# Kernel optimization log

Hardware: AMD Instinct MI355X
Metric: run time of the kernel (lower is better)

## Reference

```python
import jax, jax.numpy as jnp
import numpy as np

ALPHA = 0.2          # LeakyReLU negative slope
NEG_BIG = -9e15      # zero_vec value used before softmax masking


def setup_inputs() -> dict:
    key = jax.random.key(0)
    k1, k2, k3, k4, k5 = jax.random.split(key, 5)
    N, M, F, K = 2048, 8192, 1024, 10
    feature_matrix = jax.random.normal(k1, (N, F), dtype=jnp.float32)
    embed_matrix = jax.random.normal(k2, (M, F), dtype=jnp.float32)
    # Xavier-ish scaling for params
    weight = jax.random.normal(k3, (F, F), dtype=jnp.float32) * (1.0 / np.sqrt(F))
    a = jax.random.normal(k4, (2 * F, 1), dtype=jnp.float32) * (1.0 / np.sqrt(2 * F))
    neigh_idx = jax.random.randint(k5, (N, K), 0, M, dtype=jnp.int64)
    return {
        "feature_matrix": feature_matrix,
        "embed_matrix": embed_matrix,
        "weight": weight,
        "a": a,
        "neigh_idx": neigh_idx,
    }


def reference(feature_matrix, embed_matrix, weight, a, neigh_idx):
    # feature_matrix: [N, F] features of batch nodes
    # embed_matrix:   [M, F] features of unique sampled neighbors
    # neigh_idx:      [N, K] sampled neighbor columns (set semantics: dups collapse)
    N, F = feature_matrix.shape
    M = embed_matrix.shape[0]
    rows = jnp.arange(N)[:, None]
    mask = jnp.zeros((N, M), dtype=feature_matrix.dtype).at[rows, neigh_idx].set(1.0)

    # GAT kernel path
    hf = feature_matrix @ weight          # [N, F]
    he = embed_matrix @ weight            # [M, F]
    # e_ij = leakyrelu([h_i || h_j] . a) == leakyrelu(h_i.a1 + h_j.a2)
    a1 = a[:F, 0]
    a2 = a[F:, 0]
    e = (hf @ a1)[:, None] + (he @ a2)[None, :]          # [N, M]
    e = jnp.where(e > 0, e, ALPHA * e)                   # LeakyReLU(0.2)
    scores = jnp.where(mask > 0, e, NEG_BIG)
    attention = jax.nn.softmax(scores, axis=1)           # row softmax
    to_feats = attention @ he                            # [N, F]
    return to_feats
```

## Files before the change

kernel.cpp:

```cpp
#include <hip/hip_runtime.h>
#include <math.h>

#define ALPHA 0.2f
#define MAXK 10

typedef _Float16 half8 __attribute__((ext_vector_type(8)));
typedef _Float16 half4 __attribute__((ext_vector_type(4)));
typedef float f32x4 __attribute__((ext_vector_type(4)));

__device__ __forceinline__ void gload_lds16(const void* g, void* l) {
    __builtin_amdgcn_global_load_lds(
        (const __attribute__((address_space(1))) unsigned int*)g,
        (__attribute__((address_space(3))) unsigned int*)l, 16, 0, 0);
}

__device__ __forceinline__ float dot4(float4 a, float4 b) {
    return a.x * b.x + a.y * b.y + a.z * b.z + a.w * b.w;
}

__global__ __launch_bounds__(256) void prep_kernel(
    const float* __restrict__ W, const float* __restrict__ a,
    float* __restrict__ wa, _Float16* __restrict__ Wt, int F) {
    const int tid = threadIdx.x;
    const int nWa = F >> 2;

    if ((int)blockIdx.x >= nWa) {
        __shared__ float t[32][33];
        const int tb = blockIdx.x - nWa;
        const int tpr = F >> 5;
        const int bx = (tb % tpr) * 32;
        const int by = (tb / tpr) * 32;
        const int x = tid & 31, y = tid >> 5;
        for (int i2 = y; i2 < 32; i2 += 8)
            t[i2][x] = W[(size_t)(bx + i2) * F + by + x];
        __syncthreads();
        for (int i2 = y; i2 < 32; i2 += 8)
            Wt[(size_t)(by + i2) * F + bx + x] = (_Float16)t[x][i2];
        return;
    }

    int wave = (int)((blockIdx.x * blockDim.x + tid) >> 6);
    int lane = tid & 63;
    const float4* wr = reinterpret_cast<const float4*>(W + (size_t)wave * F);
    const float4* a1 = reinterpret_cast<const float4*>(a);
    const float4* a2 = reinterpret_cast<const float4*>(a + F);
    float acc1 = 0.f, acc2 = 0.f;
    int F4 = F >> 2;
    for (int c = lane; c < F4; c += 64) {
        float4 w = wr[c];
        acc1 += dot4(w, a1[c]);
        acc2 += dot4(w, a2[c]);
    }
    #pragma unroll
    for (int off = 32; off; off >>= 1) {
        acc1 += __shfl_down(acc1, off);
        acc2 += __shfl_down(acc2, off);
    }
    if (lane == 0) { wa[wave] = acc1; wa[F + wave] = acc2; }
}

__global__ __launch_bounds__(256) void mid_kernel(
    const float* __restrict__ feat, const float* __restrict__ embed,
    const int* __restrict__ nidx, const float* __restrict__ wa,
    _Float16* __restrict__ agg, int F) {
    const int tid = threadIdx.x;
    const int i = blockIdx.x;
    const int f = tid * 4;

    int idx[MAXK];
    bool dup[MAXK];
    #pragma unroll
    for (int k = 0; k < MAXK; k++) idx[k] = nidx[i * MAXK + k];
    #pragma unroll
    for (int k = 0; k < MAXK; k++) {
        bool d = false;
        #pragma unroll
        for (int p = 0; p < MAXK; p++)
            if (p < k) d |= (idx[p] == idx[k]);
        dup[k] = d;
    }

    float4 wa1 = *(const float4*)&wa[f];
    float4 wa2 = *(const float4*)&wa[F + f];
    float4 fv  = *(const float4*)&feat[(size_t)i * F + f];
    float a1p = dot4(fv, wa1);

    float4 rv[MAXK];
    float a2p[MAXK];
    #pragma unroll
    for (int k = 0; k < MAXK; k++) {
        rv[k] = *(const float4*)&embed[(size_t)idx[k] * F + f];
        a2p[k] = dot4(rv[k], wa2);
    }

    #pragma unroll
    for (int off = 32; off; off >>= 1) {
        a1p += __shfl_down(a1p, off);
        #pragma unroll
        for (int k = 0; k < MAXK; k++) a2p[k] += __shfl_down(a2p[k], off);
    }
    __shared__ float red[MAXK + 1][4];
    const int w = tid >> 6, l = tid & 63;
    if (l == 0) {
        red[0][w] = a1p;
        #pragma unroll
        for (int k = 0; k < MAXK; k++) red[k + 1][w] = a2p[k];
    }
    __syncthreads();

    float s1 = red[0][0] + red[0][1] + red[0][2] + red[0][3];
    float sc[MAXK];
    float m = -INFINITY;
    #pragma unroll
    for (int k = 0; k < MAXK; k++) {
        float v = s1 + red[k + 1][0] + red[k + 1][1] + red[k + 1][2] + red[k + 1][3];
        v = v > 0.f ? v : ALPHA * v;
        sc[k] = v;
        if (!dup[k]) m = fmaxf(m, v);
    }
    float sum = 0.f;
    #pragma unroll
    for (int k = 0; k < MAXK; k++) {
        sc[k] = dup[k] ? 0.f : expf(sc[k] - m);
        sum += sc[k];
    }
    float inv = 1.0f / sum;

    float4 o = make_float4(0.f, 0.f, 0.f, 0.f);
    #pragma unroll
    for (int k = 0; k < MAXK; k++) {
        float wk = sc[k] * inv;
        o.x += wk * rv[k].x;
        o.y += wk * rv[k].y;
        o.z += wk * rv[k].z;
        o.w += wk * rv[k].w;
    }
    half4 h = { (_Float16)o.x, (_Float16)o.y, (_Float16)o.z, (_Float16)o.w };
    *(half4*)&agg[(size_t)i * F + f] = h;
}

__global__ __launch_bounds__(256) void gemm_f16_kernel(
    const _Float16* __restrict__ A, const _Float16* __restrict__ Bt,
    float* __restrict__ C, int M, int N, int K) {
    __shared__ _Float16 As[2][64 * 128];
    __shared__ _Float16 Bs[2][64 * 128];
    const int tid = threadIdx.x;

    int bid = blockIdx.y * gridDim.x + blockIdx.x;
    int nwg = gridDim.x * gridDim.y;
    int cpx = nwg >> 3;
    int wg = (bid & 7) * cpx + (bid >> 3);
    const int m0 = (wg / gridDim.x) * 64;
    const int n0 = (wg % gridDim.x) * 64;

    const int l = tid & 63, wv = tid >> 6;
    const int wm = wv >> 1, wn = wv & 1;
    const int lrow = l & 15, kc = l >> 4;
    const int nt = K >> 7;

    f32x4 acc[2][2] = {};

    #define STAGE(bf, t)                                                            \
    do {                                                                            \
        int k0_ = (t) * 128;                                                        \
        _Pragma("unroll")                                                           \
        for (int j_ = 0; j_ < 4; j_++) {                                            \
            int u_ = wv * 256 + j_ * 64 + l;                                        \
            int row_ = u_ >> 4, slot_ = (u_ & 15) ^ (row_ & 7);                     \
            gload_lds16(&A[(size_t)(m0 + row_) * K + k0_ + slot_ * 8],              \
                        (void*)((char*)&As[bf][0] + u_ * 16));                      \
        }                                                                           \
        _Pragma("unroll")                                                           \
        for (int j_ = 0; j_ < 4; j_++) {                                            \
            int u_ = wv * 256 + j_ * 64 + l;                                        \
            int row_ = u_ >> 4, slot_ = (u_ & 15) ^ (row_ & 7);                     \
            gload_lds16(&Bt[(size_t)(n0 + row_) * K + k0_ + slot_ * 8],             \
                        (void*)((char*)&Bs[bf][0] + u_ * 16));                      \
        }                                                                           \
    } while (0)

    STAGE(0, 0);

    int buf = 0;
    for (int t = 0; t < nt; ++t) {
        if (t + 1 < nt) {
            STAGE(buf ^ 1, t + 1);
            asm volatile("s_waitcnt vmcnt(8)" ::: "memory");
        } else {
            asm volatile("s_waitcnt vmcnt(0)" ::: "memory");
        }
        __builtin_amdgcn_s_barrier();
        __builtin_amdgcn_sched_barrier(0);

        __builtin_amdgcn_s_setprio(1);
        #pragma unroll
        for (int ks = 0; ks < 4; ks++) {
            half8 av[2], bv[2];
            #pragma unroll
            for (int fq = 0; fq < 2; fq++) {
                int arow = wm * 32 + fq * 16 + lrow;
                int ag = (ks * 4 + kc) ^ (arow & 7);
                av[fq] = *(const half8*)((const char*)&As[buf][0] + arow * 256 + ag * 16);
                int brow = wn * 32 + fq * 16 + lrow;
                int bg = (ks * 4 + kc) ^ (brow & 7);
                bv[fq] = *(const half8*)((const char*)&Bs[buf][0] + brow * 256 + bg * 16);
            }
            #pragma unroll
            for (int fq = 0; fq < 2; fq++)
                #pragma unroll
                for (int g = 0; g < 2; g++)
                    acc[fq][g] = __builtin_amdgcn_mfma_f32_16x16x32_f16(
                        av[fq], bv[g], acc[fq][g], 0, 0, 0);
        }
        __builtin_amdgcn_s_setprio(0);

        __builtin_amdgcn_sched_barrier(0);
        __builtin_amdgcn_s_barrier();
        buf ^= 1;
    }
    #undef STAGE

    #pragma unroll
    for (int fq = 0; fq < 2; fq++)
        #pragma unroll
        for (int g = 0; g < 2; g++)
            #pragma unroll
            for (int r = 0; r < 4; r++)
                C[(size_t)(m0 + wm * 32 + fq * 16 + kc * 4 + r) * N
                  + n0 + wn * 32 + g * 16 + lrow] = acc[fq][g][r];
}

extern "C" void kernel_launch(void* const* d_in, const int* in_sizes, int n_in,
                              void* d_out, int out_size, void* d_ws, size_t ws_size,
                              hipStream_t stream) {
    const float* feat  = (const float*)d_in[0];
    const float* embed = (const float*)d_in[1];
    const float* W     = (const float*)d_in[2];
    const float* a     = (const float*)d_in[3];
    const int*   nidx  = (const int*)d_in[4];

    int F = in_sizes[3] / 2;
    int N = in_sizes[0] / F;
    int M = in_sizes[1] / F;

    float* ws = (float*)d_ws;
    float* wa = ws;
    _Float16* agg_f16 = (_Float16*)(wa + 2 * F);
    _Float16* wt_f16  = agg_f16 + (size_t)N * F;
    (void)M;

    {
        int nWa = F / 4;
        int nT  = (F / 32) * (F / 32);
        prep_kernel<<<nWa + nT, 256, 0, stream>>>(W, a, wa, wt_f16, F);
    }
    mid_kernel<<<N, 256, 0, stream>>>(feat, embed, nidx, wa, agg_f16, F);
    {
        dim3 grid(F / 64, N / 64);
        gemm_f16_kernel<<<grid, 256, 0, stream>>>(agg_f16, wt_f16, (float*)d_out, N, F, F);
    }
}
```

Before: 37.25 us.

## Overlap second-half aggregation with first-half GEMM in a combined kernel

Splits the rows into two halves. The first half is aggregated by mid_kernel. A combo kernel then runs the GEMM for the first half in some blocks while other blocks aggregate the second half, and a final GEMM covers the second half. The aim is to fill the machine by letting gather-bound aggregation and MFMA-bound GEMM run concurrently. The cost is an extra launch, and the combo kernel reserves 32KB of LDS per block, which may lower occupancy for the aggregation blocks.

```diff
diff --git a/kernel.cpp b/kernel.cpp
--- a/kernel.cpp
+++ b/kernel.cpp
@@ -17,13 +17,158 @@
 __device__ __forceinline__ float dot4(float4 a, float4 b) {
     return a.x * b.x + a.y * b.y + a.z * b.z + a.w * b.w;
 }
+
+
+__device__ __forceinline__ void mid_body(
+    int i, int tid, const float* __restrict__ feat, const float* __restrict__ embed,
+    const int* __restrict__ nidx, const float* __restrict__ wa,
+    _Float16* __restrict__ agg, int F, char* smem) {
+    const int f = tid * 4;
+    int idx[MAXK];
+    bool dup[MAXK];
+    #pragma unroll
+    for (int k = 0; k < MAXK; k++) idx[k] = nidx[i * MAXK + k];
+    #pragma unroll
+    for (int k = 0; k < MAXK; k++) {
+        bool d = false;
+        #pragma unroll
+        for (int p = 0; p < MAXK; p++)
+            if (p < k) d |= (idx[p] == idx[k]);
+        dup[k] = d;
+    }
+    float4 wa1 = *(const float4*)&wa[f];
+    float4 wa2 = *(const float4*)&wa[F + f];
+    float4 fv  = *(const float4*)&feat[(size_t)i * F + f];
+    float a1p = dot4(fv, wa1);
+    float4 rv[MAXK];
+    float a2p[MAXK];
+    #pragma unroll
+    for (int k = 0; k < MAXK; k++) {
+        rv[k] = *(const float4*)&embed[(size_t)idx[k] * F + f];
+        a2p[k] = dot4(rv[k], wa2);
+    }
+    #pragma unroll
+    for (int off = 32; off; off >>= 1) {
+        a1p += __shfl_down(a1p, off);
+        #pragma unroll
+        for (int k = 0; k < MAXK; k++) a2p[k] += __shfl_down(a2p[k], off);
+    }
+    float (*red)[4] = (float(*)[4])smem;
+    const int w = tid >> 6, l = tid & 63;
+    if (l == 0) {
+        red[0][w] = a1p;
+        #pragma unroll
+        for (int k = 0; k < MAXK; k++) red[k + 1][w] = a2p[k];
+    }
+    __syncthreads();
+    float s1 = red[0][0] + red[0][1] + red[0][2] + red[0][3];
+    float sc[MAXK];
+    float m = -INFINITY;
+    #pragma unroll
+    for (int k = 0; k < MAXK; k++) {
+        float v = s1 + red[k + 1][0] + red[k + 1][1] + red[k + 1][2] + red[k + 1][3];
+        v = v > 0.f ? v : ALPHA * v;
+        sc[k] = v;
+        if (!dup[k]) m = fmaxf(m, v);
+    }
+    float sum = 0.f;
+    #pragma unroll
+    for (int k = 0; k < MAXK; k++) {
+        sc[k] = dup[k] ? 0.f : expf(sc[k] - m);
+        sum += sc[k];
+    }
+    float inv = 1.0f / sum;
+    float4 o = make_float4(0.f, 0.f, 0.f, 0.f);
+    #pragma unroll
+    for (int k = 0; k < MAXK; k++) {
+        float wk = sc[k] * inv;
+        o.x += wk * rv[k].x;
+        o.y += wk * rv[k].y;
+        o.z += wk * rv[k].z;
+        o.w += wk * rv[k].w;
+    }
+    half4 h = { (_Float16)o.x, (_Float16)o.y, (_Float16)o.z, (_Float16)o.w };
+    *(half4*)&agg[(size_t)i * F + f] = h;
+}
+
+__device__ __forceinline__ void gemm64_body(
+    int m0, int n0, int tid, const _Float16* __restrict__ A,
+    const _Float16* __restrict__ Bt, float* __restrict__ C,
+    int K, int Nc, char* smem) {
+    char* AsB = smem;
+    char* BsB = smem + 16384;
+    const int l = tid & 63, wv = tid >> 6;
+    const int wm = wv >> 1, wn = wv & 1;
+    const int lrow = l & 15, kc = l >> 4;
+    const int srow = l >> 3;
+    const int sslot = (l & 7) ^ (srow & 7);
+    const int nt = K >> 6;
+    const int rg0 = wv * 2, rg1 = wv * 2 + 1;
+    f32x4 acc[2][2] = {};
+
+    #define GSTAGE(bf, t_)                                                         \
+    do {                                                                           \
+        int k0_ = (t_) * 64;                                                       \
+        gload_lds16(&A[(size_t)(m0 + rg0 * 8 + srow) * K + k0_ + sslot * 8],       \
+                    (void*)(AsB + (bf) * 8192 + rg0 * 1024 + l * 16));             \
+        gload_lds16(&A[(size_t)(m0 + rg1 * 8 + srow) * K + k0_ + sslot * 8],       \
+                    (void*)(AsB + (bf) * 8192 + rg1 * 1024 + l * 16));             \
+        gload_lds16(&Bt[(size_t)(n0 + rg0 * 8 + srow) * K + k0_ + sslot * 8],      \
+                    (void*)(BsB + (bf) * 8192 + rg0 * 1024 + l * 16));             \
+        gload_lds16(&Bt[(size_t)(n0 + rg1 * 8 + srow) * K + k0_ + sslot * 8],      \
+                    (void*)(BsB + (bf) * 8192 + rg1 * 1024 + l * 16));             \
+    } while (0)
+
+    GSTAGE(0, 0);
+    asm volatile("s_waitcnt vmcnt(0)" ::: "memory");
+    __syncthreads();
+
+    int buf = 0;
+    for (int t = 0; t < nt; ++t) {
+        if (t + 1 < nt) GSTAGE(buf ^ 1, t + 1);
+        half8 av[2][2], bv[2][2];
+        #pragma unroll
+        for (int ks = 0; ks < 2; ks++) {
+            #pragma unroll
+            for (int fq = 0; fq < 2; fq++) {
+                int arow = wm * 32 + fq * 16 + lrow;
+                int aslot = (ks * 4 + kc) ^ (arow & 7);
+                av[ks][fq] = *(const half8*)(AsB + buf * 8192 + arow * 128 + aslot * 16);
+                int brow = wn * 32 + fq * 16 + lrow;
+                int bslot = (ks * 4 + kc) ^ (brow & 7);
+                bv[ks][fq] = *(const half8*)(BsB + buf * 8192 + brow * 128 + bslot * 16);
+            }
+        }
+        #pragma unroll
+        for (int ks = 0; ks < 2; ks++)
+            #pragma unroll
+            for (int fq = 0; fq < 2; fq++)
+                #pragma unroll
+                for (int g2 = 0; g2 < 2; g2++)
+                    acc[fq][g2] = __builtin_amdgcn_mfma_f32_16x16x32_f16(
+                        av[ks][fq], bv[ks][g2], acc[fq][g2], 0, 0, 0);
+        asm volatile("s_waitcnt vmcnt(0)" ::: "memory");
+        __syncthreads();
+        buf ^= 1;
+    }
+    #undef GSTAGE
+
+    #pragma unroll
+    for (int fq = 0; fq < 2; fq++)
+        #pragma unroll
+        for (int g2 = 0; g2 < 2; g2++)
+            #pragma unroll
+            for (int r = 0; r < 4; r++)
+                C[(size_t)(m0 + wm * 32 + fq * 16 + kc * 4 + r) * Nc
+                  + n0 + wn * 32 + g2 * 16 + lrow] = acc[fq][g2][r];
+}
+
 
 __global__ __launch_bounds__(256) void prep_kernel(
     const float* __restrict__ W, const float* __restrict__ a,
     float* __restrict__ wa, _Float16* __restrict__ Wt, int F) {
     const int tid = threadIdx.x;
     const int nWa = F >> 2;
-
     if ((int)blockIdx.x >= nWa) {
         __shared__ float t[32][33];
         const int tb = blockIdx.x - nWa;
@@ -38,7 +183,6 @@
             Wt[(size_t)(by + i2) * F + bx + x] = (_Float16)t[x][i2];
         return;
     }
-
     int wave = (int)((blockIdx.x * blockDim.x + tid) >> 6);
     int lane = tid & 63;
     const float4* wr = reinterpret_cast<const float4*>(W + (size_t)wave * F);
@@ -63,85 +207,34 @@
     const float* __restrict__ feat, const float* __restrict__ embed,
     const int* __restrict__ nidx, const float* __restrict__ wa,
     _Float16* __restrict__ agg, int F) {
+    __shared__ __align__(16) char smem[192];
+    mid_body(blockIdx.x, threadIdx.x, feat, embed, nidx, wa, agg, F, smem);
+}
+
+__global__ __launch_bounds__(256) void combo_kernel(
+    const float* __restrict__ feat, const float* __restrict__ embed,
+    const int* __restrict__ nidx, const float* __restrict__ wa,
+    const _Float16* __restrict__ agg_c, _Float16* __restrict__ agg,
+    const _Float16* __restrict__ Wt, float* __restrict__ C, int F, int halfN) {
+    __shared__ __align__(16) char smem[32768];
     const int tid = threadIdx.x;
-    const int i = blockIdx.x;
-    const int f = tid * 4;
-
-    int idx[MAXK];
-    bool dup[MAXK];
-    #pragma unroll
-    for (int k = 0; k < MAXK; k++) idx[k] = nidx[i * MAXK + k];
-    #pragma unroll
-    for (int k = 0; k < MAXK; k++) {
-        bool d = false;
-        #pragma unroll
-        for (int p = 0; p < MAXK; p++)
-            if (p < k) d |= (idx[p] == idx[k]);
-        dup[k] = d;
-    }
-
-    float4 wa1 = *(const float4*)&wa[f];
-    float4 wa2 = *(const float4*)&wa[F + f];
-    float4 fv  = *(const float4*)&feat[(size_t)i * F + f];
-    float a1p = dot4(fv, wa1);
-
-    float4 rv[MAXK];
-    float a2p[MAXK];
-    #pragma unroll
-    for (int k = 0; k < MAXK; k++) {
-        rv[k] = *(const float4*)&embed[(size_t)idx[k] * F + f];
-        a2p[k] = dot4(rv[k], wa2);
-    }
-
-    #pragma unroll
-    for (int off = 32; off; off >>= 1) {
-        a1p += __shfl_down(a1p, off);
-        #pragma unroll
-        for (int k = 0; k < MAXK; k++) a2p[k] += __shfl_down(a2p[k], off);
-    }
-    __shared__ float red[MAXK + 1][4];
-    const int w = tid >> 6, l = tid & 63;
-    if (l == 0) {
-        red[0][w] = a1p;
-        #pragma unroll
-        for (int k = 0; k < MAXK; k++) red[k + 1][w] = a2p[k];
-    }
-    __syncthreads();
-
-    float s1 = red[0][0] + red[0][1] + red[0][2] + red[0][3];
-    float sc[MAXK];
-    float m = -INFINITY;
-    #pragma unroll
-    for (int k = 0; k < MAXK; k++) {
-        float v = s1 + red[k + 1][0] + red[k + 1][1] + red[k + 1][2] + red[k + 1][3];
-        v = v > 0.f ? v : ALPHA * v;
-        sc[k] = v;
-        if (!dup[k]) m = fmaxf(m, v);
-    }
-    float sum = 0.f;
-    #pragma unroll
-    for (int k = 0; k < MAXK; k++) {
-        sc[k] = dup[k] ? 0.f : expf(sc[k] - m);
-        sum += sc[k];
-    }
-    float inv = 1.0f / sum;
-
-    float4 o = make_float4(0.f, 0.f, 0.f, 0.f);
-    #pragma unroll
-    for (int k = 0; k < MAXK; k++) {
-        float wk = sc[k] * inv;
-        o.x += wk * rv[k].x;
-        o.y += wk * rv[k].y;
-        o.z += wk * rv[k].z;
-        o.w += wk * rv[k].w;
-    }
-    half4 h = { (_Float16)o.x, (_Float16)o.y, (_Float16)o.z, (_Float16)o.w };
-    *(half4*)&agg[(size_t)i * F + f] = h;
+    const int bid = blockIdx.x;
+    const int nG = (halfN >> 6) * (F >> 6);
+
+    if (bid < nG) {
+        int cpx = nG >> 3;
+        int g = (bid & 7) * cpx + (bid >> 3);
+        int m0 = (g >> 4) * 64;
+        int n0 = (g & 15) * 64;
+        gemm64_body(m0, n0, tid, agg_c, Wt, C, F, F, smem);
+        return;
+    }
+    mid_body(halfN + (bid - nG), tid, feat, embed, nidx, wa, agg, F, smem);
 }
 
 __global__ __launch_bounds__(256) void gemm_f16_kernel(
     const _Float16* __restrict__ A, const _Float16* __restrict__ Bt,
-    float* __restrict__ C, int M, int N, int K) {
+    float* __restrict__ C, int mOff, int N, int K) {
     __shared__ _Float16 As[2][64 * 128];
     __shared__ _Float16 Bs[2][64 * 128];
     const int tid = threadIdx.x;
@@ -150,7 +243,7 @@
     int nwg = gridDim.x * gridDim.y;
     int cpx = nwg >> 3;
     int wg = (bid & 7) * cpx + (bid >> 3);
-    const int m0 = (wg / gridDim.x) * 64;
+    const int m0 = mOff + (wg / gridDim.x) * 64;
     const int n0 = (wg % gridDim.x) * 64;
 
     const int l = tid & 63, wv = tid >> 6;
@@ -242,11 +335,13 @@
     int F = in_sizes[3] / 2;
     int N = in_sizes[0] / F;
     int M = in_sizes[1] / F;
+    int halfN = N / 2;
 
     float* ws = (float*)d_ws;
     float* wa = ws;
     _Float16* agg_f16 = (_Float16*)(wa + 2 * F);
     _Float16* wt_f16  = agg_f16 + (size_t)N * F;
+    float* C = (float*)d_out;
     (void)M;
 
     {
@@ -254,9 +349,15 @@
         int nT  = (F / 32) * (F / 32);
         prep_kernel<<<nWa + nT, 256, 0, stream>>>(W, a, wa, wt_f16, F);
     }
-    mid_kernel<<<N, 256, 0, stream>>>(feat, embed, nidx, wa, agg_f16, F);
+    mid_kernel<<<halfN, 256, 0, stream>>>(feat, embed, nidx, wa, agg_f16, F);
     {
-        dim3 grid(F / 64, N / 64);
-        gemm_f16_kernel<<<grid, 256, 0, stream>>>(agg_f16, wt_f16, (float*)d_out, N, F, F);
-    }
-}
+        int nG = (halfN / 64) * (F / 64);
+        combo_kernel<<<nG + halfN, 256, 0, stream>>>(feat, embed, nidx, wa,
+                                                     agg_f16, agg_f16, wt_f16,
+                                                     C, F, halfN);
+    }
+    {
+        dim3 grid(F / 64, halfN / 64);
+        gemm_f16_kernel<<<grid, 256, 0, stream>>>(agg_f16, wt_f16, C, halfN, F, F);
+    }
+}
```

Measured after the change: 44.29 us. 1.19x slower.
